# Kernel tuning notes

Measured on AMD Instinct MI355X. Metric: run time of the kernel, lower is better.

Reference implementation:

```python
import jax, jax.numpy as jnp
import numpy as np

A = 8732          # SSD300 anchor count
C = 91            # num classes (incl. background at index 0)
B = 32
IMG = 300.0
SCORE_THRESH = 0.01
NMS_THRESH = 0.45
TOPK = 400        # topk_candidates per class
MAX_DET = 200     # detections_per_img
BBOX_XY_W = 10.0  # box_coder weights (10,10,5,5)
BBOX_WH_W = 5.0
BBOX_CLIP = float(np.log(1000.0 / 16.0))


def setup_inputs() -> dict:
    key = jax.random.key(0)
    k1, k2, kc, ks = jax.random.split(key, 4)
    cls_logits = jax.random.normal(k1, (B, A, C), jnp.float32)
    bbox_regression = jax.random.normal(k2, (B, A, 4), jnp.float32)
    # plausible anchors in xyxy on a 300x300 image
    cxcy = jax.random.uniform(kc, (A, 2), minval=0.0, maxval=IMG)
    wh = jax.random.uniform(ks, (A, 2), minval=10.0, maxval=150.0)
    anchors = jnp.concatenate([cxcy - wh / 2, cxcy + wh / 2], axis=-1)
    return {"cls_logits": cls_logits, "bbox_regression": bbox_regression, "anchors": anchors}


def decode_boxes(rel, anchors):
    wa = anchors[:, 2] - anchors[:, 0]
    ha = anchors[:, 3] - anchors[:, 1]
    cxa = anchors[:, 0] + 0.5 * wa
    cya = anchors[:, 1] + 0.5 * ha
    dx = rel[:, 0] / BBOX_XY_W
    dy = rel[:, 1] / BBOX_XY_W
    dw = jnp.minimum(rel[:, 2] / BBOX_WH_W, BBOX_CLIP)
    dh = jnp.minimum(rel[:, 3] / BBOX_WH_W, BBOX_CLIP)
    cx = dx * wa + cxa
    cy = dy * ha + cya
    w = jnp.exp(dw) * wa
    h = jnp.exp(dh) * ha
    boxes = jnp.stack([cx - 0.5 * w, cy - 0.5 * h, cx + 0.5 * w, cy + 0.5 * h], axis=-1)
    return jnp.clip(boxes, 0.0, IMG)


def iou_one_vs_all(box, boxes):
    # box [4], boxes [N,4] -> [N]
    lt = jnp.maximum(box[:2], boxes[:, :2])
    rb = jnp.minimum(box[2:], boxes[:, 2:])
    wh = jnp.clip(rb - lt, 0.0)
    inter = wh[:, 0] * wh[:, 1]
    a1 = (box[2] - box[0]) * (box[3] - box[1])
    a2 = (boxes[:, 2] - boxes[:, 0]) * (boxes[:, 3] - boxes[:, 1])
    return inter / (a1 + a2 - inter + 1e-9)


def greedy_nms(boxes, scores, iou_thresh, max_det):
    # boxes [N,4] (class-offset), scores [N] (-inf = invalid). Returns top max_det keep idxs.
    def step(sc, _):
        i = jnp.argmax(sc)
        best_sc = sc[i]
        iou = iou_one_vs_all(boxes[i], boxes)
        sc = jnp.where(iou > iou_thresh, -jnp.inf, sc)
        sc = sc.at[i].set(-jnp.inf)
        return sc, (i, best_sc)
    _, (keep, kept_sc) = jax.lax.scan(step, scores, None, length=max_det)
    return keep, kept_sc


def postprocess_one(logits, rel, anchors):
    scores = jax.nn.softmax(logits, axis=-1)      # [A,C]
    boxes = decode_boxes(rel, anchors)            # [A,4]
    fg = scores[:, 1:].T                          # [C-1, A], skip background
    masked = jnp.where(fg > SCORE_THRESH, fg, -jnp.inf)
    top_sc, top_idx = jax.lax.top_k(masked, TOPK)  # [C-1, TOPK]
    cand_boxes = boxes[top_idx].reshape(-1, 4)     # [(C-1)*TOPK, 4]
    cand_sc = top_sc.reshape(-1)
    labels = jnp.broadcast_to(jnp.arange(1, C, dtype=jnp.int32)[:, None], (C - 1, TOPK)).reshape(-1)
    # batched_nms: offset boxes per class so different classes never overlap
    offset = labels.astype(boxes.dtype) * (IMG + 1.0)
    keep, kept_sc = greedy_nms(cand_boxes + offset[:, None], cand_sc, NMS_THRESH, MAX_DET)
    valid = jnp.isfinite(kept_sc)
    out_boxes = jnp.where(valid[:, None], cand_boxes[keep], 0.0)
    out_scores = jnp.where(valid, kept_sc, 0.0)
    out_labels = jnp.where(valid, labels[keep], 0)
    return out_boxes, out_scores, out_labels


def reference(cls_logits, bbox_regression, anchors):
    # returns (boxes [B,200,4], scores [B,200], labels [B,200] int32); invalid slots zeroed
    return jax.vmap(lambda l, r: postprocess_one(l, r, anchors))(cls_logits, bbox_regression)
```

## Files before the change

### kernel.cpp

```cpp
#include <hip/hip_runtime.h>
#include <hip/hip_bf16.h>
#include <cstdint>
#include <cstddef>
#include <math.h>

#pragma clang fp contract(off)

#define A_N 8732
#define C_N 91
#define CM1 90
#define B_N 32
#define TOPK 400
#define MAXDET 200
#define NT 512
#define CCAP 1024
#define BBOX_CLIPF 4.135166556742356f

#define IOU_M ((double)0.45f + 0x1p-26)

typedef float f4u __attribute__((ext_vector_type(4), aligned(4)));

__device__ __forceinline__ float ldin(const void* p, size_t i, int isbf16) {
    if (isbf16) return __bfloat162float(((const __hip_bfloat16*)p)[i]);
    return ((const float*)p)[i];
}

__device__ __forceinline__ float np_expf(float x) {
    float q = rintf(x * 1.442695040f);
    float r = fmaf(q, -0.693359375f, x);
    r = fmaf(q, 2.12194440e-4f, r);
    float p = 1.9875691500E-4f;
    p = fmaf(p, r, 1.3981999507E-3f);
    p = fmaf(p, r, 8.3334519073E-3f);
    p = fmaf(p, r, 4.1665795894E-2f);
    p = fmaf(p, r, 1.6666665459E-1f);
    p = fmaf(p, r, 5.0000001201E-1f);
    p = fmaf(p, r, 1.0f);
    p = fmaf(p, r, 1.0f);
    return ldexpf(p, (int)q);
}

__global__ void k_sniff(const unsigned* __restrict__ words, int* __restrict__ flag) {
    __shared__ int cnt_s;
    if (threadIdx.x == 0) cnt_s = 0;
    __syncthreads();
    int local = 0;
    for (int i = threadIdx.x; i < 4096; i += 256) {
        unsigned w = words[i];
        unsigned e = (w >> 7) & 0xFFu;
        if (e >= 100u && e <= 140u) local++;
    }
    atomicAdd(&cnt_s, local);
    __syncthreads();
    if (threadIdx.x == 0) flag[0] = (cnt_s > 2048) ? 1 : 0;
}

__global__ void k_stats(const void* __restrict__ logits,
                        const void* __restrict__ rel,
                        const void* __restrict__ anchors,
                        const int* __restrict__ flag,
                        float* __restrict__ amax,
                        float* __restrict__ denom,
                        float* __restrict__ boxes,
                        unsigned* __restrict__ scT) {
    int i = blockIdx.x * blockDim.x + threadIdx.x;
    if (i >= B_N * A_N) return;
    int bf = flag[0];
    size_t base = (size_t)i * C_N;
    int bb = i / A_N, aa = i - bb * A_N;
    unsigned* sbase = scT ? (scT + (size_t)bb * CM1 * A_N + aa) : (unsigned*)0;

    if (!bf) {
        const float* lp = (const float*)logits + base;
        float x[91];
        #pragma unroll
        for (int k = 0; k < 22; ++k) {
            f4u v = *(const f4u*)(lp + 4 * k);
            x[4 * k + 0] = v.x; x[4 * k + 1] = v.y;
            x[4 * k + 2] = v.z; x[4 * k + 3] = v.w;
        }
        x[88] = lp[88]; x[89] = lp[89]; x[90] = lp[90];

        float m = -INFINITY;
        #pragma unroll
        for (int c = 0; c < 91; ++c) m = fmaxf(m, x[c]);

        #pragma unroll
        for (int c = 0; c < 91; ++c) x[c] = np_expf(x[c] - m);

        float r[8];
        #pragma unroll
        for (int j = 0; j < 8; ++j) {
            float s = x[j];
            #pragma unroll
            for (int k = 1; k < 11; ++k) s += x[8 * k + j];
            r[j] = s;
        }
        float res = ((r[0] + r[1]) + (r[2] + r[3])) + ((r[4] + r[5]) + (r[6] + r[7]));
        res += x[88]; res += x[89]; res += x[90];
        amax[i]  = m;
        denom[i] = res;

        if (sbase) {
            #pragma unroll
            for (int c = 1; c < 91; ++c) {
                float sc = x[c] / res;
                sbase[(size_t)(c - 1) * A_N] =
                    (sc > 0.01f) ? __float_as_uint(sc) : 0u;
            }
        }
    } else {
        float m = -INFINITY;
        for (int c = 0; c < C_N; ++c) m = fmaxf(m, ldin(logits, base + c, bf));
        float r[8];
        for (int j = 0; j < 8; ++j) r[j] = np_expf(ldin(logits, base + j, bf) - m);
        for (int c = 8; c < 88; c += 8)
            for (int j = 0; j < 8; ++j) r[j] += np_expf(ldin(logits, base + c + j, bf) - m);
        float res = ((r[0] + r[1]) + (r[2] + r[3])) + ((r[4] + r[5]) + (r[6] + r[7]));
        res += np_expf(ldin(logits, base + 88, bf) - m);
        res += np_expf(ldin(logits, base + 89, bf) - m);
        res += np_expf(ldin(logits, base + 90, bf) - m);
        amax[i]  = m;
        denom[i] = res;
        if (sbase) {
            for (int c = 1; c < C_N; ++c) {
                float sc = np_expf(ldin(logits, base + c, bf) - m) / res;
                sbase[(size_t)(c - 1) * A_N] =
                    (sc > 0.01f) ? __float_as_uint(sc) : 0u;
            }
        }
    }

    {
        int a = aa;
        float ax1, ay1, ax2, ay2, r0, r1, r2, r3;
        if (!bf) {
            float4 av = ((const float4*)anchors)[a];
            float4 rv = ((const float4*)rel)[i];
            ax1 = av.x; ay1 = av.y; ax2 = av.z; ay2 = av.w;
            r0 = rv.x; r1 = rv.y; r2 = rv.z; r3 = rv.w;
        } else {
            ax1 = ldin(anchors, (size_t)a * 4 + 0, bf);
            ay1 = ldin(anchors, (size_t)a * 4 + 1, bf);
            ax2 = ldin(anchors, (size_t)a * 4 + 2, bf);
            ay2 = ldin(anchors, (size_t)a * 4 + 3, bf);
            r0 = ldin(rel, (size_t)i * 4 + 0, bf);
            r1 = ldin(rel, (size_t)i * 4 + 1, bf);
            r2 = ldin(rel, (size_t)i * 4 + 2, bf);
            r3 = ldin(rel, (size_t)i * 4 + 3, bf);
        }
        float wa = ax2 - ax1, ha = ay2 - ay1;
        float cxa = ax1 + 0.5f * wa, cya = ay1 + 0.5f * ha;
        float dx = r0 / 10.0f, dy = r1 / 10.0f;
        float dw = fminf(r2 / 5.0f, BBOX_CLIPF);
        float dh = fminf(r3 / 5.0f, BBOX_CLIPF);
        float cx = dx * wa + cxa, cy = dy * ha + cya;
        float w = np_expf(dw) * wa, h = np_expf(dh) * ha;
        float4 o;
        o.x = fminf(fmaxf(cx - 0.5f * w, 0.0f), 300.0f);
        o.y = fminf(fmaxf(cy - 0.5f * h, 0.0f), 300.0f);
        o.z = fminf(fmaxf(cx + 0.5f * w, 0.0f), 300.0f);
        o.w = fminf(fmaxf(cy + 0.5f * h, 0.0f), 300.0f);
        ((float4*)boxes)[i] = o;
    }
}

__global__ __launch_bounds__(NT) void k_topknms_pre(const unsigned* __restrict__ scT,
                                                    const float* __restrict__ boxes,
                                                    unsigned long long* __restrict__ kkey,
                                                    int* __restrict__ kcnt) {
    __shared__ __align__(16) float4 nbq[TOPK];
    __shared__ float sar[TOPK];
    __shared__ unsigned long long wlist[512];
    __shared__ unsigned long long cand[CCAP];
    __shared__ unsigned hist[1024];
    __shared__ unsigned long long fsup[8];
    __shared__ unsigned long long ksv[8];
    __shared__ unsigned sel_b;
    __shared__ int sel_rem;
    __shared__ int nreal_s;
    __shared__ int eqlist[64];
    __shared__ int eqn, nsel, candn, total_s;

    int bc = blockIdx.x;
    int b  = bc / CM1;
    int cm = bc % CM1;
    int t  = threadIdx.x;

    const unsigned* srow = scT + (size_t)bc * A_N;
    const uint4* srow4 = (const uint4*)srow;

    if (t == 0) { eqn = 0; nsel = 0; candn = 0; total_s = 0; }
    for (int q = t; q < 1024; q += NT) hist[q] = 0u;
    __syncthreads();
    for (int k = t; k < A_N / 4; k += NT) {
        uint4 v = srow4[k];
        if (v.x) atomicAdd(&hist[(v.x >> 16) & 0x3FFu], 1u);
        if (v.y) atomicAdd(&hist[(v.y >> 16) & 0x3FFu], 1u);
        if (v.z) atomicAdd(&hist[(v.z >> 16) & 0x3FFu], 1u);
        if (v.w) atomicAdd(&hist[(v.w >> 16) & 0x3FFu], 1u);
    }
    __syncthreads();

    if (t < 64) {
        unsigned s = 0;
        #pragma unroll
        for (int q = 0; q < 16; ++q) s += hist[16 * t + q];
        unsigned suf = s;
        for (int o = 1; o < 64; o <<= 1) {
            unsigned vv = __shfl_down(suf, o);
            if (t + o < 64) suf += vv;
        }
        if (t == 0) nreal_s = (int)suf;
        unsigned cum = suf - s;
        for (int q = 15; q >= 0; --q) {
            unsigned h = hist[16 * t + q];
            if ((int)cum < TOPK && TOPK <= (int)(cum + h)) {
                sel_b = (unsigned)(16 * t + q);
                sel_rem = TOPK - (int)cum;
            }
            cum += h;
        }
    }
    __syncthreads();
    int nreal = nreal_s;
    bool sel_path = (nreal >= TOPK);
    unsigned selL1 = sel_b;
    unsigned prefix1 = (0xFu << 10) | selL1;
    __syncthreads();

    if (sel_path) { for (int q = t; q < 1024; q += NT) hist[q] = 0u; }
    __syncthreads();
    for (int k = t; k < A_N / 4; k += NT) {
        uint4 vv = srow4[k];
        unsigned va[4] = {vv.x, vv.y, vv.z, vv.w};
        #pragma unroll
        for (int c = 0; c < 4; ++c) {
            unsigned v = va[c];
            if (!v) continue;
            unsigned a = (unsigned)(4 * k + c);
            if (sel_path) {
                unsigned bkt = (v >> 16) & 0x3FFu;
                if (bkt > selL1) {
                    int slot = atomicAdd(&nsel, 1);
                    if (slot < 512)
                        wlist[slot] = ((unsigned long long)v << 32) | (unsigned)(~a);
                } else if (bkt == selL1) {
                    int s2 = atomicAdd(&candn, 1);
                    if (s2 < CCAP)
                        cand[s2] = ((unsigned long long)v << 32) | (unsigned)(~a);
                    atomicAdd(&hist[(v >> 6) & 0x3FFu], 1u);
                }
            } else {
                int slot = atomicAdd(&nsel, 1);
                if (slot < 512)
                    wlist[slot] = ((unsigned long long)v << 32) | (unsigned)(~a);
            }
        }
    }
    __syncthreads();

    if (sel_path) {
        int ngt = nsel;
        int cn  = candn;
        bool fast = (cn <= CCAP) && (ngt + cn <= 512);
        if (fast) {
            for (int q = t; q < cn; q += NT) wlist[ngt + q] = cand[q];
            __syncthreads();
            if (t == 0) nsel = ngt + cn;
            __syncthreads();
        } else {
            bool ovf = (cn > CCAP);
            if (t < 64) {
                int rem = sel_rem;
                unsigned s = 0;
                #pragma unroll
                for (int q = 0; q < 16; ++q) s += hist[16 * t + q];
                unsigned suf = s;
                for (int o = 1; o < 64; o <<= 1) {
                    unsigned vv = __shfl_down(suf, o);
                    if (t + o < 64) suf += vv;
                }
                unsigned cum = suf - s;
                for (int q = 15; q >= 0; --q) {
                    unsigned h = hist[16 * t + q];
                    if ((int)cum < rem && rem <= (int)(cum + h)) {
                        sel_b = (unsigned)(16 * t + q);
                        sel_rem = rem - (int)cum;
                    }
                    cum += h;
                }
            }
            __syncthreads();
            unsigned prefix2 = (prefix1 << 10) | sel_b;

            if (t < 64) hist[t] = 0u;
            __syncthreads();
            if (!ovf) {
                int cc = cn < CCAP ? cn : CCAP;
                for (int q = t; q < cc; q += NT) {
                    unsigned v = (unsigned)(cand[q] >> 32);
                    if ((v >> 6) == prefix2) atomicAdd(&hist[v & 0x3Fu], 1u);
                }
            } else {
                for (int a = t; a < A_N; a += NT) {
                    unsigned v = srow[a];
                    if (v && (v >> 6) == prefix2) atomicAdd(&hist[v & 0x3Fu], 1u);
                }
            }
            __syncthreads();
            if (t == 0) {
                int rem = sel_rem;
                unsigned cum = 0;
                for (int bq = 63; bq >= 0; --bq) {
                    unsigned h = hist[bq];
                    if ((int)cum < rem && rem <= (int)(cum + h)) {
                        sel_b = (unsigned)bq;
                        sel_rem = rem - (int)cum;
                        break;
                    }
                    cum += h;
                }
            }
            __syncthreads();
            unsigned sstar = (prefix2 << 6) | sel_b;
            int teq = sel_rem;

            if (!ovf) {
                int cc = cn < CCAP ? cn : CCAP;
                for (int q = t; q < cc; q += NT) {
                    unsigned long long cv = cand[q];
                    unsigned v = (unsigned)(cv >> 32);
                    if (v > sstar) {
                        int slot = atomicAdd(&nsel, 1);
                        if (slot < 512) wlist[slot] = cv;
                    } else if (v == sstar) {
                        int s2 = atomicAdd(&eqn, 1);
                        if (s2 < 64) eqlist[s2] = (int)(~(unsigned)cv);
                    }
                }
            } else {
                for (int a = t; a < A_N; a += NT) {
                    unsigned v = srow[a];
                    if (!v) continue;
                    if ((v >> 16) == prefix1) {
                        if (v > sstar) {
                            int slot = atomicAdd(&nsel, 1);
                            if (slot < 512)
                                wlist[slot] = ((unsigned long long)v << 32) |
                                              (unsigned)(~(unsigned)a);
                        } else if (v == sstar) {
                            int s2 = atomicAdd(&eqn, 1);
                            if (s2 < 64) eqlist[s2] = a;
                        }
                    }
                }
            }
            __syncthreads();
            if (t == 0) {
                int n = eqn < 64 ? eqn : 64;
                for (int i2 = 1; i2 < n; ++i2) {
                    int v2 = eqlist[i2], j2 = i2 - 1;
                    while (j2 >= 0 && eqlist[j2] > v2) { eqlist[j2 + 1] = eqlist[j2]; --j2; }
                    eqlist[j2 + 1] = v2;
                }
                int tq = teq < n ? teq : n;
                int bse = nsel;
                for (int q2 = 0; q2 < tq; ++q2) {
                    int slot = bse + q2;
                    if (slot < 512)
                        wlist[slot] = ((unsigned long long)sstar << 32) |
                                      (unsigned)(~(unsigned)eqlist[q2]);
                }
                nsel = bse + tq;
            }
            __syncthreads();
        }
    }
    int ns = nsel < 512 ? nsel : 512;
    if (t >= ns) wlist[t] = 0ull;
    __syncthreads();

    {
        unsigned long long u = wlist[t];
        for (int k = 2; k <= 512; k <<= 1) {
            bool up = ((t & k) == 0);
            for (int j = k >> 1; j >= 64; j >>= 1) {
                __syncthreads();
                wlist[t] = u;
                __syncthreads();
                unsigned long long v = wlist[t ^ j];
                bool takeMax = (((t & j) == 0) == up);
                u = takeMax ? (u > v ? u : v) : (u < v ? u : v);
            }
            for (int j = ((k >> 1) < 64 ? (k >> 1) : 32); j > 0; j >>= 1) {
                unsigned long long v = __shfl_xor(u, j);
                bool takeMax = (((t & j) == 0) == up);
                u = takeMax ? (u > v ? u : v) : (u < v ? u : v);
            }
        }
        __syncthreads();
        wlist[t] = u;
        __syncthreads();
    }

    int m = ns < TOPK ? ns : TOPK;
    float offc = (float)(cm + 1) * 301.0f;
    if (t < m) {
        unsigned aidx = ~(unsigned)(wlist[t] & 0xFFFFFFFFull);
        const float* bp = boxes + ((size_t)b * A_N + aidx) * 4;
        float4 q;
        q.x = bp[0] + offc; q.y = bp[1] + offc;
        q.z = bp[2] + offc; q.w = bp[3] + offc;
        nbq[t] = q;
        sar[t] = (q.z - q.x) * (q.w - q.y);
    }
    if (t < 8) { fsup[t] = 0ull; ksv[t] = 0ull; }
    __syncthreads();

    int nch = (m + 63) >> 6;
    for (int g = 0; g < nch; ++g) {
        if (t < 64) {
            int bse = 64 * g;
            int jmax = m - bse; if (jmax > 64) jmax = 64;
            bool valid = t < jmax;
            float4 cb = valid ? nbq[bse + t] : make_float4(0.f, 0.f, 0.f, 0.f);
            float car = valid ? sar[bse + t] : 0.0f;
            unsigned long long sup = fsup[g], kv = 0ull;
            unsigned long long rem =
                ((jmax == 64) ? ~0ull : ((1ull << jmax) - 1ull)) & ~sup;
            while (rem) {
                int j = __builtin_ctzll(rem);
                float rx1 = __shfl(cb.x, j), ry1 = __shfl(cb.y, j);
                float rx2 = __shfl(cb.z, j), ry2 = __shfl(cb.w, j);
                float ra  = __shfl(car, j);
                bool p = false;
                if (valid && t > j) {
                    float lx = fmaxf(rx1, cb.x), ly = fmaxf(ry1, cb.y);
                    float rx = fminf(rx2, cb.z), ry = fminf(ry2, cb.w);
                    float ww = fmaxf(rx - lx, 0.0f), hh = fmaxf(ry - ly, 0.0f);
                    float inter = ww * hh;
                    float U = ra + car - inter + 1e-9f;
                    p = ((double)inter > IOU_M * (double)U);
                }
                unsigned long long wj = __ballot(p);
                kv |= 1ull << j;
                sup |= wj;
                rem &= ~(sup | (1ull << j));
            }
            if (t == 0) { ksv[g] = kv; total_s += __popcll(kv); }
        }
        __syncthreads();
        if (total_s >= MAXDET) break;
        if (g + 1 < nch) {
            int w = t >> 6, l = t & 63;
            int h = g + 1 + w;
            if (h < nch) {
                unsigned long long kv = ksv[g];
                int jmax2 = m - 64 * h; if (jmax2 > 64) jmax2 = 64;
                bool v2 = l < jmax2;
                float4 cbl = v2 ? nbq[64 * h + l] : make_float4(0.f, 0.f, 0.f, 0.f);
                float cal = v2 ? sar[64 * h + l] : 0.0f;
                bool acc = false;
                unsigned long long rr = kv;
                while (rr) {
                    int r = __builtin_ctzll(rr); rr &= rr - 1;
                    float4 rq = nbq[64 * g + r];
                    float rar = sar[64 * g + r];
                    if (v2 && !acc) {
                        float lx = fmaxf(rq.x, cbl.x), ly = fmaxf(rq.y, cbl.y);
                        float rx = fminf(rq.z, cbl.z), ry = fminf(rq.w, cbl.w);
                        float ww = fmaxf(rx - lx, 0.0f), hh = fmaxf(ry - ly, 0.0f);
                        float inter = ww * hh;
                        float U = rar + cal - inter + 1e-9f;
                        acc = ((double)inter > IOU_M * (double)U);
                    }
                }
                unsigned long long wd = __ballot(acc);
                if (l == 0) fsup[h] |= wd;
            }
        }
        __syncthreads();
    }

    if (t < 64) {
        int l = t, basek = 0;
        for (int g = 0; g < nch; ++g) {
            unsigned long long kv = ksv[g];
            int row = 64 * g + l;
            if ((kv >> l) & 1ull) {
                int rank = basek + __popcll(kv & ((1ull << l) - 1ull));
                if (rank < MAXDET) {
                    unsigned long long wv = wlist[row];
                    unsigned sbts = (unsigned)(wv >> 32);
                    unsigned aa2  = ~(unsigned)wv;
                    int flat = cm * TOPK + row;
                    unsigned long long key =
                        ((unsigned long long)sbts << 31) |
                        ((unsigned long long)(131071 - flat) << 14) |
                        (unsigned long long)aa2;
                    kkey[(size_t)bc * MAXDET + rank] = key;
                }
            }
            basek += __popcll(kv);
        }
        if (l == 0) kcnt[bc] = total_s < MAXDET ? total_s : MAXDET;
    }
}

__global__ __launch_bounds__(NT) void k_topknms(const void* __restrict__ logits,
                                                const int* __restrict__ flag,
                                                const float* __restrict__ amax,
                                                const float* __restrict__ denom,
                                                const float* __restrict__ boxes,
                                                unsigned long long* __restrict__ kkey,
                                                int* __restrict__ kcnt) {
    __shared__ union {
        unsigned sbits[A_N];
        unsigned long long msk[TOPK * 7];
    } su;
    __shared__ unsigned long long wlist[512];
    __shared__ float bx1[TOPK], by1[TOPK], bx2[TOPK], by2[TOPK], bar[TOPK];
    __shared__ int wred[NT / 64];
    __shared__ unsigned bcast_p;
    __shared__ int bcast_rem;
    __shared__ int eqlist[64];
    __shared__ int eqn;
    __shared__ int bcast_athr;
    __shared__ int nsel;

    int bc = blockIdx.x;
    int b  = bc / CM1;
    int cm = bc % CM1;
    int bf = flag[0];
    int t  = threadIdx.x;

    for (int a = t; a < A_N; a += NT) {
        size_t base = (size_t)b * A_N + a;
        float e  = np_expf(ldin(logits, base * C_N + (cm + 1), bf) - amax[base]);
        float sc = e / denom[base];
        su.sbits[a] = (sc > 0.01f) ? __float_as_uint(sc) : 0u;
    }
    if (t == 0) { eqn = 0; nsel = 0; }
    __syncthreads();

    {
        int c0 = 0;
        for (int a = t; a < A_N; a += NT) c0 += (su.sbits[a] != 0u);
        for (int o = 32; o; o >>= 1) c0 += __shfl_down(c0, o);
        if ((t & 63) == 0) wred[t >> 6] = c0;
        __syncthreads();
        if (t == 0) {
            int tot = 0;
            for (int wv = 0; wv < NT / 64; ++wv) tot += wred[wv];
            bcast_rem = tot;
        }
        __syncthreads();
    }
    int nreal = bcast_rem;
    __syncthreads();

    unsigned sstar = 0u;
    int teq = 0;
    if (nreal >= TOPK) {
        unsigned p = 0x3C000000u;
        int rem = TOPK;
        for (int bit = 25; bit >= 0; --bit) {
            unsigned q = p | (1u << bit);
            int cnt = 0;
            for (int a = t; a < A_N; a += NT) cnt += ((su.sbits[a] >> bit) == (q >> bit));
            for (int o = 32; o; o >>= 1) cnt += __shfl_down(cnt, o);
            if ((t & 63) == 0) wred[t >> 6] = cnt;
            __syncthreads();
            if (t == 0) {
                int tot = 0;
                for (int wv = 0; wv < NT / 64; ++wv) tot += wred[wv];
                if (tot >= rem) { bcast_p = q; bcast_rem = rem; }
                else            { bcast_p = p; bcast_rem = rem - tot; }
            }
            __syncthreads();
            p = bcast_p; rem = bcast_rem;
            __syncthreads();
        }
        sstar = p;
        teq = rem;
        for (int a = t; a < A_N; a += NT) {
            if (su.sbits[a] == sstar) {
                int slot = atomicAdd(&eqn, 1);
                if (slot < 64) eqlist[slot] = a;
            }
        }
        __syncthreads();
        if (t == 0) {
            int n = eqn < 64 ? eqn : 64;
            for (int i = 1; i < n; ++i) {
                int v = eqlist[i], j = i - 1;
                while (j >= 0 && eqlist[j] > v) { eqlist[j + 1] = eqlist[j]; --j; }
                eqlist[j + 1] = v;
            }
            int tq = teq < n ? teq : n;
            bcast_athr = (tq > 0) ? eqlist[tq - 1] : -1;
        }
        __syncthreads();
    }
    int athr = (nreal >= TOPK) ? bcast_athr : -1;
    __syncthreads();

    for (int a = t; a < A_N; a += NT) {
        unsigned v = su.sbits[a];
        bool sel;
        if (nreal >= TOPK)
            sel = (v > sstar) || (v == sstar && a <= athr);
        else
            sel = (v != 0u);
        if (sel) {
            int slot = atomicAdd(&nsel, 1);
            if (slot < 512)
                wlist[slot] = ((unsigned long long)v << 32) | (unsigned)(~(unsigned)a);
        }
    }
    __syncthreads();
    int ns = nsel < 512 ? nsel : 512;
    if (t < 512 && t >= ns) wlist[t] = 0ull;
    __syncthreads();

    for (int k = 2; k <= 512; k <<= 1) {
        for (int j = k >> 1; j > 0; j >>= 1) {
            int ixj = t ^ j;
            if (ixj > t) {
                unsigned long long u = wlist[t], v = wlist[ixj];
                bool desc = ((t & k) == 0);
                if (desc ? (u < v) : (u > v)) { wlist[t] = v; wlist[ixj] = u; }
            }
            __syncthreads();
        }
    }

    int m = ns < TOPK ? ns : TOPK;
    float offc = (float)(cm + 1) * 301.0f;
    if (t < m) {
        unsigned aidx = ~(unsigned)(wlist[t] & 0xFFFFFFFFull);
        const float* bp = boxes + ((size_t)b * A_N + aidx) * 4;
        float x1 = bp[0] + offc, y1 = bp[1] + offc;
        float x2 = bp[2] + offc, y2 = bp[3] + offc;
        bx1[t] = x1; by1[t] = y1; bx2[t] = x2; by2[t] = y2;
        bar[t] = (x2 - x1) * (y2 - y1);
    }
    __syncthreads();

    if (t < m) {
        unsigned long long w[7] = {0, 0, 0, 0, 0, 0, 0};
        float x1 = bx1[t], y1 = by1[t], x2 = bx2[t], y2 = by2[t], a1 = bar[t];
        for (int j = t + 1; j < m; ++j) {
            float lx = fmaxf(x1, bx1[j]), ly = fmaxf(y1, by1[j]);
            float rx = fminf(x2, bx2[j]), ry = fminf(y2, by2[j]);
            float ww = fmaxf(rx - lx, 0.0f), hh = fmaxf(ry - ly, 0.0f);
            float inter = ww * hh;
            float iou = inter / (a1 + bar[j] - inter + 1e-9f);
            if (iou > 0.45f) w[j >> 6] |= 1ull << (j & 63);
        }
        for (int k2 = 0; k2 < 7; ++k2) su.msk[t * 7 + k2] = w[k2];
    }
    __syncthreads();

    if (t == 0) {
        unsigned long long sup[7] = {0, 0, 0, 0, 0, 0, 0};
        int cnt = 0;
        for (int i = 0; i < m; ++i) {
            if (!((sup[i >> 6] >> (i & 63)) & 1ull)) {
                unsigned long long wv = wlist[i];
                unsigned sb2 = (unsigned)(wv >> 32);
                unsigned a  = ~(unsigned)wv;
                int flat = cm * TOPK + i;
                unsigned long long key =
                    ((unsigned long long)sb2 << 31) |
                    ((unsigned long long)(131071 - flat) << 14) |
                    (unsigned long long)a;
                kkey[(size_t)bc * MAXDET + cnt] = key;
                cnt++;
                if (cnt == MAXDET) break;
                const unsigned long long* r = &su.msk[i * 7];
                for (int k2 = 0; k2 < 7; ++k2) sup[k2] |= r[k2];
            }
        }
        kcnt[bc] = cnt;
    }
}

__global__ __launch_bounds__(256) void k_merge(const unsigned long long* __restrict__ kkey,
                                               const int* __restrict__ kcnt,
                                               const float* __restrict__ boxes,
                                               float* __restrict__ out) {
    __shared__ unsigned hist[1024];
    __shared__ unsigned long long wl[256];
    __shared__ int kc[CM1];
    __shared__ int tot_s;
    __shared__ unsigned selb_s, selh_s;
    __shared__ int selrem_s;
    __shared__ int gcnt;
    __shared__ unsigned long long T_s;

    int b = blockIdx.x;
    int t = threadIdx.x;
    const unsigned long long* keys = kkey + (size_t)b * (CM1 * MAXDET);
    const float* bx = boxes + (size_t)b * A_N * 4;
    float* ob = out + (size_t)b * MAXDET * 4;
    float* os = out + (size_t)B_N * MAXDET * 4 + (size_t)b * MAXDET;
    float* ol = out + (size_t)B_N * MAXDET * 5 + (size_t)b * MAXDET;

    if (t < CM1) kc[t] = kcnt[b * CM1 + t];
    if (t == 0) { gcnt = 0; T_s = 0ull; }
    __syncthreads();
    if (t == 0) {
        int tot = 0;
        for (int c = 0; c < CM1; ++c) tot += kc[c];
        tot_s = tot;
        selrem_s = MAXDET;
    }
    __syncthreads();
    int total = tot_s;

    if (total > MAXDET) {
        unsigned long long prefix = 0ull;
        for (int l = 0; l < 7; ++l) {
            int width = (l == 6) ? 2 : 10;
            int shift = (l == 6) ? 0 : (52 - 10 * l);
            int nb = 1 << width;
            for (int q = t; q < nb; q += 256) hist[q] = 0u;
            __syncthreads();
            for (int idx = t; idx < CM1 * MAXDET; idx += 256) {
                int c = idx / MAXDET;
                if (idx - c * MAXDET < kc[c]) {
                    unsigned long long key = keys[idx];
                    if ((key >> (shift + width)) == prefix)
                        atomicAdd(&hist[(unsigned)(key >> shift) & (unsigned)(nb - 1)], 1u);
                }
            }
            __syncthreads();
            if (nb >= 64) {
                if (t < 64) {
                    int rem = selrem_s;
                    int per = nb / 64;
                    unsigned s = 0;
                    for (int q = 0; q < per; ++q) s += hist[per * t + q];
                    unsigned suf = s;
                    for (int o = 1; o < 64; o <<= 1) {
                        unsigned vv = __shfl_down(suf, o);
                        if (t + o < 64) suf += vv;
                    }
                    unsigned cum = suf - s;
                    for (int q = per - 1; q >= 0; --q) {
                        unsigned h = hist[per * t + q];
                        if ((int)cum < rem && rem <= (int)(cum + h)) {
                            selb_s = (unsigned)(per * t + q);
                            selrem_s = rem - (int)cum;
                            selh_s = h;
                        }
                        cum += h;
                    }
                }
            } else if (t == 0) {
                int rem = selrem_s;
                unsigned cum = 0;
                for (int bq = nb - 1; bq >= 0; --bq) {
                    unsigned h = hist[bq];
                    if ((int)cum < rem && rem <= (int)(cum + h)) {
                        selb_s = (unsigned)bq;
                        selrem_s = rem - (int)cum;
                        selh_s = h;
                        break;
                    }
                    cum += h;
                }
            }
            __syncthreads();
            prefix = (prefix << width) | (unsigned long long)selb_s;
            bool whole = (selrem_s == (int)selh_s);
            __syncthreads();
            if (whole || l == 6) {
                if (t == 0) T_s = prefix << shift;
                break;
            }
        }
        __syncthreads();
    }
    unsigned long long T = T_s;

    wl[t] = 0ull;
    __syncthreads();
    for (int idx = t; idx < CM1 * MAXDET; idx += 256) {
        int c = idx / MAXDET;
        if (idx - c * MAXDET < kc[c]) {
            unsigned long long key = keys[idx];
            if (total <= MAXDET ? true : (key >= T)) {
                int s = atomicAdd(&gcnt, 1);
                if (s < 256) wl[s] = key;
            }
        }
    }
    __syncthreads();

    for (int k = 2; k <= 256; k <<= 1) {
        for (int j = k >> 1; j > 0; j >>= 1) {
            int ixj = t ^ j;
            if (ixj > t) {
                unsigned long long u = wl[t], v = wl[ixj];
                bool desc = ((t & k) == 0);
                if (desc ? (u < v) : (u > v)) { wl[t] = v; wl[ixj] = u; }
            }
            __syncthreads();
        }
    }

    if (t < MAXDET) {
        unsigned long long key = wl[t];
        if (key == 0ull) {
            ob[t * 4 + 0] = 0.0f; ob[t * 4 + 1] = 0.0f;
            ob[t * 4 + 2] = 0.0f; ob[t * 4 + 3] = 0.0f;
            os[t] = 0.0f; ol[t] = 0.0f;
        } else {
            int a = (int)(key & 0x3FFFull);
            int flat = 131071 - (int)((key >> 14) & 0x1FFFFull);
            int cmv = flat / TOPK;
            const float* bp = bx + (size_t)a * 4;
            ob[t * 4 + 0] = bp[0]; ob[t * 4 + 1] = bp[1];
            ob[t * 4 + 2] = bp[2]; ob[t * 4 + 3] = bp[3];
            os[t] = __uint_as_float((unsigned)(key >> 31));
            ol[t] = (float)(cmv + 1);
        }
    }
}

extern "C" void kernel_launch(void* const* d_in, const int* in_sizes, int n_in,
                              void* d_out, int out_size, void* d_ws, size_t ws_size,
                              hipStream_t stream) {
    const void* logits  = d_in[0];
    const void* rel     = d_in[1];
    const void* anchors = d_in[2];
    float* out = (float*)d_out;

    char* ws = (char*)d_ws;
    size_t off = 0;
    auto alloc = [&](size_t bytes) -> void* {
        void* p = ws + off;
        off = (off + bytes + 255) & ~(size_t)255;
        return p;
    };
    float* boxes  = (float*)alloc((size_t)B_N * A_N * 4 * sizeof(float));
    float* amax   = (float*)alloc((size_t)B_N * A_N * sizeof(float));
    float* denom  = (float*)alloc((size_t)B_N * A_N * sizeof(float));
    int*   flag   = (int*)alloc(256);
    unsigned long long* kkey = (unsigned long long*)alloc((size_t)B_N * CM1 * MAXDET * sizeof(unsigned long long));
    int* kcnt     = (int*)alloc((size_t)B_N * CM1 * sizeof(int));

    size_t scT_bytes = (size_t)B_N * CM1 * A_N * sizeof(unsigned);
    unsigned* scT = nullptr;
    if (off + scT_bytes <= ws_size) scT = (unsigned*)alloc(scT_bytes);

    int gridBA = (B_N * A_N + 255) / 256;

    k_sniff<<<1, 256, 0, stream>>>((const unsigned*)logits, flag);
    k_stats<<<gridBA, 256, 0, stream>>>(logits, rel, anchors, flag, amax, denom, boxes, scT);
    if (scT)
        k_topknms_pre<<<B_N * CM1, NT, 0, stream>>>(scT, boxes, kkey, kcnt);
    else
        k_topknms<<<B_N * CM1, NT, 0, stream>>>(logits, flag, amax, denom, boxes, kkey, kcnt);
    k_merge<<<B_N, 256, 0, stream>>>(kkey, kcnt, boxes, out);
}
```

Baseline: 555.3 us.

## Recompute softmax exps from reloads, cache score rows in registers, restructure NMS cross-chunk suppression

k_stats no longer holds 91 logits in a register array. It reloads the logits and recomputes exp for the max, sum and score-write passes, cutting register pressure at the cost of extra exp work and L1/L2 reads. The top-k kernel keeps its score row in registers between the two histogram passes instead of reading global memory twice. NMS now computes cross-chunk suppression lazily at the start of each chunk, one wave per earlier chunk, using atomicOr, instead of eagerly after each chunk. The merge kernel launches with 512 threads.

```diff
diff --git a/kernel.cpp b/kernel.cpp
--- a/kernel.cpp
+++ b/kernel.cpp
@@ -13,6 +13,7 @@
 #define TOPK 400
 #define MAXDET 200
 #define NT 512
+#define NIT 5
 #define CCAP 1024
 #define BBOX_CLIPF 4.135166556742356f
 
@@ -72,42 +73,58 @@
 
     if (!bf) {
         const float* lp = (const float*)logits + base;
-        float x[91];
+
+        float m = -INFINITY;
         #pragma unroll
         for (int k = 0; k < 22; ++k) {
             f4u v = *(const f4u*)(lp + 4 * k);
-            x[4 * k + 0] = v.x; x[4 * k + 1] = v.y;
-            x[4 * k + 2] = v.z; x[4 * k + 3] = v.w;
-        }
-        x[88] = lp[88]; x[89] = lp[89]; x[90] = lp[90];
-
-        float m = -INFINITY;
+            m = fmaxf(m, v.x); m = fmaxf(m, v.y); m = fmaxf(m, v.z); m = fmaxf(m, v.w);
+        }
+        m = fmaxf(m, lp[88]); m = fmaxf(m, lp[89]); m = fmaxf(m, lp[90]);
+
+        float r[8];
+        {
+            f4u v0 = *(const f4u*)(lp);
+            f4u v1 = *(const f4u*)(lp + 4);
+            r[0] = np_expf(v0.x - m); r[1] = np_expf(v0.y - m);
+            r[2] = np_expf(v0.z - m); r[3] = np_expf(v0.w - m);
+            r[4] = np_expf(v1.x - m); r[5] = np_expf(v1.y - m);
+            r[6] = np_expf(v1.z - m); r[7] = np_expf(v1.w - m);
+        }
         #pragma unroll
-        for (int c = 0; c < 91; ++c) m = fmaxf(m, x[c]);
-
-        #pragma unroll
-        for (int c = 0; c < 91; ++c) x[c] = np_expf(x[c] - m);
-
-        float r[8];
-        #pragma unroll
-        for (int j = 0; j < 8; ++j) {
-            float s = x[j];
-            #pragma unroll
-            for (int k = 1; k < 11; ++k) s += x[8 * k + j];
-            r[j] = s;
+        for (int k = 1; k < 11; ++k) {
+            f4u v0 = *(const f4u*)(lp + 8 * k);
+            f4u v1 = *(const f4u*)(lp + 8 * k + 4);
+            r[0] += np_expf(v0.x - m); r[1] += np_expf(v0.y - m);
+            r[2] += np_expf(v0.z - m); r[3] += np_expf(v0.w - m);
+            r[4] += np_expf(v1.x - m); r[5] += np_expf(v1.y - m);
+            r[6] += np_expf(v1.z - m); r[7] += np_expf(v1.w - m);
         }
         float res = ((r[0] + r[1]) + (r[2] + r[3])) + ((r[4] + r[5]) + (r[6] + r[7]));
-        res += x[88]; res += x[89]; res += x[90];
+        res += np_expf(lp[88] - m);
+        res += np_expf(lp[89] - m);
+        res += np_expf(lp[90] - m);
         amax[i]  = m;
         denom[i] = res;
 
         if (sbase) {
             #pragma unroll
-            for (int c = 1; c < 91; ++c) {
-                float sc = x[c] / res;
-                sbase[(size_t)(c - 1) * A_N] =
-                    (sc > 0.01f) ? __float_as_uint(sc) : 0u;
-            }
+            for (int k = 0; k < 22; ++k) {
+                f4u v = *(const f4u*)(lp + 1 + 4 * k);
+                float s0 = np_expf(v.x - m) / res;
+                float s1 = np_expf(v.y - m) / res;
+                float s2 = np_expf(v.z - m) / res;
+                float s3 = np_expf(v.w - m) / res;
+                size_t o = (size_t)(4 * k) * A_N;
+                sbase[o]                    = (s0 > 0.01f) ? __float_as_uint(s0) : 0u;
+                sbase[o + (size_t)A_N]      = (s1 > 0.01f) ? __float_as_uint(s1) : 0u;
+                sbase[o + (size_t)2 * A_N]  = (s2 > 0.01f) ? __float_as_uint(s2) : 0u;
+                sbase[o + (size_t)3 * A_N]  = (s3 > 0.01f) ? __float_as_uint(s3) : 0u;
+            }
+            float s89 = np_expf(lp[89] - m) / res;
+            float s90 = np_expf(lp[90] - m) / res;
+            sbase[(size_t)88 * A_N] = (s89 > 0.01f) ? __float_as_uint(s89) : 0u;
+            sbase[(size_t)89 * A_N] = (s90 > 0.01f) ? __float_as_uint(s90) : 0u;
         }
     } else {
         float m = -INFINITY;
@@ -190,15 +207,21 @@
     const unsigned* srow = scT + (size_t)bc * A_N;
     const uint4* srow4 = (const uint4*)srow;
 
+    uint4 st[NIT];
     if (t == 0) { eqn = 0; nsel = 0; candn = 0; total_s = 0; }
     for (int q = t; q < 1024; q += NT) hist[q] = 0u;
     __syncthreads();
-    for (int k = t; k < A_N / 4; k += NT) {
-        uint4 v = srow4[k];
-        if (v.x) atomicAdd(&hist[(v.x >> 16) & 0x3FFu], 1u);
-        if (v.y) atomicAdd(&hist[(v.y >> 16) & 0x3FFu], 1u);
-        if (v.z) atomicAdd(&hist[(v.z >> 16) & 0x3FFu], 1u);
-        if (v.w) atomicAdd(&hist[(v.w >> 16) & 0x3FFu], 1u);
+    #pragma unroll
+    for (int it = 0; it < NIT; ++it) {
+        int k = t + it * NT;
+        if (k < A_N / 4) {
+            uint4 v = srow4[k];
+            st[it] = v;
+            if (v.x) atomicAdd(&hist[(v.x >> 16) & 0x3FFu], 1u);
+            if (v.y) atomicAdd(&hist[(v.y >> 16) & 0x3FFu], 1u);
+            if (v.z) atomicAdd(&hist[(v.z >> 16) & 0x3FFu], 1u);
+            if (v.w) atomicAdd(&hist[(v.w >> 16) & 0x3FFu], 1u);
+        }
     }
     __syncthreads();
 
@@ -231,8 +254,11 @@
 
     if (sel_path) { for (int q = t; q < 1024; q += NT) hist[q] = 0u; }
     __syncthreads();
-    for (int k = t; k < A_N / 4; k += NT) {
-        uint4 vv = srow4[k];
+    #pragma unroll
+    for (int it = 0; it < NIT; ++it) {
+        int k = t + it * NT;
+        if (k >= A_N / 4) continue;
+        uint4 vv = st[it];
         unsigned va[4] = {vv.x, vv.y, vv.z, vv.w};
         #pragma unroll
         for (int c = 0; c < 4; ++c) {
@@ -420,6 +446,33 @@
 
     int nch = (m + 63) >> 6;
     for (int g = 0; g < nch; ++g) {
+        if (g > 0) {
+            int w = t >> 6, l = t & 63;
+            if (w < g) {
+                int jmax2 = m - 64 * g; if (jmax2 > 64) jmax2 = 64;
+                bool v2 = l < jmax2;
+                float4 cbl = v2 ? nbq[64 * g + l] : make_float4(0.f, 0.f, 0.f, 0.f);
+                float cal = v2 ? sar[64 * g + l] : 0.0f;
+                bool acc = false;
+                unsigned long long rr = ksv[w];
+                while (rr) {
+                    int r = __builtin_ctzll(rr); rr &= rr - 1;
+                    float4 rq = nbq[64 * w + r];
+                    float rar = sar[64 * w + r];
+                    if (v2 && !acc) {
+                        float lx = fmaxf(rq.x, cbl.x), ly = fmaxf(rq.y, cbl.y);
+                        float rx = fminf(rq.z, cbl.z), ry = fminf(rq.w, cbl.w);
+                        float ww = fmaxf(rx - lx, 0.0f), hh = fmaxf(ry - ly, 0.0f);
+                        float inter = ww * hh;
+                        float U = rar + cal - inter + 1e-9f;
+                        acc = ((double)inter > IOU_M * (double)U);
+                    }
+                }
+                unsigned long long wd = __ballot(acc);
+                if (l == 0 && wd) atomicOr(&fsup[g], wd);
+            }
+            __syncthreads();
+        }
         if (t < 64) {
             int bse = 64 * g;
             int jmax = m - bse; if (jmax > 64) jmax = 64;
@@ -452,35 +505,6 @@
         }
         __syncthreads();
         if (total_s >= MAXDET) break;
-        if (g + 1 < nch) {
-            int w = t >> 6, l = t & 63;
-            int h = g + 1 + w;
-            if (h < nch) {
-                unsigned long long kv = ksv[g];
-                int jmax2 = m - 64 * h; if (jmax2 > 64) jmax2 = 64;
-                bool v2 = l < jmax2;
-                float4 cbl = v2 ? nbq[64 * h + l] : make_float4(0.f, 0.f, 0.f, 0.f);
-                float cal = v2 ? sar[64 * h + l] : 0.0f;
-                bool acc = false;
-                unsigned long long rr = kv;
-                while (rr) {
-                    int r = __builtin_ctzll(rr); rr &= rr - 1;
-                    float4 rq = nbq[64 * g + r];
-                    float rar = sar[64 * g + r];
-                    if (v2 && !acc) {
-                        float lx = fmaxf(rq.x, cbl.x), ly = fmaxf(rq.y, cbl.y);
-                        float rx = fminf(rq.z, cbl.z), ry = fminf(rq.w, cbl.w);
-                        float ww = fmaxf(rx - lx, 0.0f), hh = fmaxf(ry - ly, 0.0f);
-                        float inter = ww * hh;
-                        float U = rar + cal - inter + 1e-9f;
-                        acc = ((double)inter > IOU_M * (double)U);
-                    }
-                }
-                unsigned long long wd = __ballot(acc);
-                if (l == 0) fsup[h] |= wd;
-            }
-        }
-        __syncthreads();
     }
 
     if (t < 64) {
@@ -687,7 +711,7 @@
     }
 }
 
-__global__ __launch_bounds__(256) void k_merge(const unsigned long long* __restrict__ kkey,
+__global__ __launch_bounds__(512) void k_merge(const unsigned long long* __restrict__ kkey,
                                                const int* __restrict__ kcnt,
                                                const float* __restrict__ boxes,
                                                float* __restrict__ out) {
@@ -726,9 +750,9 @@
             int width = (l == 6) ? 2 : 10;
             int shift = (l == 6) ? 0 : (52 - 10 * l);
             int nb = 1 << width;
-            for (int q = t; q < nb; q += 256) hist[q] = 0u;
-            __syncthreads();
-            for (int idx = t; idx < CM1 * MAXDET; idx += 256) {
+            for (int q = t; q < nb; q += 512) hist[q] = 0u;
+            __syncthreads();
+            for (int idx = t; idx < CM1 * MAXDET; idx += 512) {
                 int c = idx / MAXDET;
                 if (idx - c * MAXDET < kc[c]) {
                     unsigned long long key = keys[idx];
@@ -786,9 +810,9 @@
     }
     unsigned long long T = T_s;
 
-    wl[t] = 0ull;
-    __syncthreads();
-    for (int idx = t; idx < CM1 * MAXDET; idx += 256) {
+    if (t < 256) wl[t] = 0ull;
+    __syncthreads();
+    for (int idx = t; idx < CM1 * MAXDET; idx += 512) {
         int c = idx / MAXDET;
         if (idx - c * MAXDET < kc[c]) {
             unsigned long long key = keys[idx];
@@ -802,11 +826,13 @@
 
     for (int k = 2; k <= 256; k <<= 1) {
         for (int j = k >> 1; j > 0; j >>= 1) {
-            int ixj = t ^ j;
-            if (ixj > t) {
-                unsigned long long u = wl[t], v = wl[ixj];
-                bool desc = ((t & k) == 0);
-                if (desc ? (u < v) : (u > v)) { wl[t] = v; wl[ixj] = u; }
+            if (t < 256) {
+                int ixj = t ^ j;
+                if (ixj > t) {
+                    unsigned long long u = wl[t], v = wl[ixj];
+                    bool desc = ((t & k) == 0);
+                    if (desc ? (u < v) : (u > v)) { wl[t] = v; wl[ixj] = u; }
+                }
             }
             __syncthreads();
         }
@@ -865,5 +891,5 @@
         k_topknms_pre<<<B_N * CM1, NT, 0, stream>>>(scT, boxes, kkey, kcnt);
     else
         k_topknms<<<B_N * CM1, NT, 0, stream>>>(logits, flag, amax, denom, boxes, kkey, kcnt);
-    k_merge<<<B_N, 256, 0, stream>>>(kkey, kcnt, boxes, out);
+    k_merge<<<B_N, 512, 0, stream>>>(kkey, kcnt, boxes, out);
 }
```

After: 584.4 us. +5.3%, slower.
